# Kernel tuning notes

Measured on AMD Instinct MI355X. Metric: run time of the kernel, lower is better.

The kernel has to match this reference:

```python
import jax, jax.numpy as jnp
import numpy as np
import math

B, P, N = 4, 8, 512
D_MODEL, H, D_K = 128, 4, 32
T_ALL = 4
WHICH_IDX = np.array([0, 1, 3])  # which_transition_matrices = [T,T,F,T]
T = 3
EPS = 1e-5


def setup_inputs() -> dict:
    key = jax.random.key(0)
    ks = jax.random.split(key, 12)
    inputs = jax.random.normal(ks[0], (B, P, N, D_MODEL), jnp.float32)
    c_inputs = jax.random.normal(ks[1], (B, P, N, D_MODEL), jnp.float32)
    vals = jax.random.uniform(ks[2], (T_ALL, N, N), jnp.float32)
    keep = (jax.random.uniform(ks[3], (T_ALL, N, N)) < 0.05).astype(jnp.float32)
    eye = jnp.eye(N, dtype=jnp.float32)
    transition_matrices = vals * keep * (1.0 - eye) + eye
    s = 1.0 / math.sqrt(D_MODEL)
    Wq = jax.random.normal(ks[4], (T, D_MODEL, D_MODEL), jnp.float32) * s
    Wk = jax.random.normal(ks[5], (T, D_MODEL, D_MODEL), jnp.float32) * s
    Wv = jax.random.normal(ks[6], (T, D_MODEL, D_MODEL), jnp.float32) * s
    Wo = jax.random.normal(ks[7], (D_MODEL, T * D_MODEL), jnp.float32) * (1.0 / math.sqrt(T * D_MODEL))
    ln_gamma = jnp.ones((D_MODEL,), jnp.float32)
    ln_beta = jnp.zeros((D_MODEL,), jnp.float32)
    return dict(inputs=inputs, c_inputs=c_inputs, transition_matrices=transition_matrices,
                Wq=Wq, Wk=Wk, Wv=Wv, Wo=Wo, ln_gamma=ln_gamma, ln_beta=ln_beta)


def reference(inputs, c_inputs, transition_matrices, Wq, Wk, Wv, Wo, ln_gamma, ln_beta):
    tm = transition_matrices[jnp.asarray(WHICH_IDX)]  # [T, N, N]
    # per-transition-matrix projections (torch Linear: x @ W.T), then split heads
    def proj(W):
        y = jnp.einsum('bpnd,tod->tbpno', inputs, W)
        return y.reshape(T, B, P, N, H, D_K)
    Q, K, V = proj(Wq), proj(Wk), proj(Wv)
    scores = jnp.einsum('tbpnhk,tbpmhk->tbphnm', Q, K) / math.sqrt(D_K)
    mask = jnp.where(tm != 0, 0.0, -jnp.inf)[:, None, None, None]  # [T,1,1,1,N,N]
    alpha = jax.nn.softmax(scores + mask, axis=-1)
    # post-softmax reweighting by transition matrix, then V matmul
    out = jnp.einsum('tbphnm,tbpmhk->tbpnhk', alpha * tm[:, None, None, None], V)
    out = out.reshape(T, B, P, N, D_MODEL)
    out = jnp.moveaxis(out, 0, -2).reshape(B, P, N, T * D_MODEL)  # concat over matrices
    out = jnp.einsum('bpnf,df->bpnd', out, Wo)  # final Linear (bias=False); dropout p=0
    res = out + inputs
    mu = res.mean(-1, keepdims=True)
    var = ((res - mu) ** 2).mean(-1, keepdims=True)
    return (res - mu) / jnp.sqrt(var + EPS) * ln_gamma + ln_beta
```

## Files before the change

kernel.cpp:

```cpp
#include <hip/hip_runtime.h>


typedef __attribute__((ext_vector_type(8))) short  short8;
typedef __attribute__((ext_vector_type(4))) float  floatx4;

#define WS_BIG   50331648ull
#define WS_XL    54919168ull
#define QSCALE   0.25503486f

__device__ __forceinline__ float b2f(unsigned short u) {
    union { unsigned int i; float f; } v; v.i = ((unsigned int)u) << 16; return v.f;
}
__device__ __forceinline__ unsigned short f2b(float f) {
    union { float f; unsigned int i; } v; v.f = f;
    unsigned int x = v.i;
    return (unsigned short)((x + 0x7fffu + ((x >> 16) & 1u)) >> 16);
}
__device__ __forceinline__ short8 cvt8(const float* p) {
    floatx4 a = *(const floatx4*)p;
    floatx4 b = *(const floatx4*)(p + 4);
    short8 r;
    r[0] = (short)f2b(a[0]); r[1] = (short)f2b(a[1]);
    r[2] = (short)f2b(a[2]); r[3] = (short)f2b(a[3]);
    r[4] = (short)f2b(b[0]); r[5] = (short)f2b(b[1]);
    r[6] = (short)f2b(b[2]); r[7] = (short)f2b(b[3]);
    return r;
}

__global__ __launch_bounds__(256) void k_prep(
    const float* __restrict__ X,  const float* __restrict__ Wq,
    const float* __restrict__ Wk, const float* __restrict__ Wv,
    const float* __restrict__ Wo,
    unsigned short* __restrict__ Xb, unsigned short* __restrict__ Wb,
    unsigned short* __restrict__ Wob)
{
    size_t i = ((size_t)blockIdx.x * 256 + threadIdx.x) * 8;
    const float* src; unsigned short* dst; size_t off;
    if      (i < 2097152) { src = X;  dst = Xb;          off = i; }
    else if (i < 2146304) { src = Wq; dst = Wb;          off = i - 2097152; }
    else if (i < 2195456) { src = Wk; dst = Wb + 49152;  off = i - 2146304; }
    else if (i < 2244608) { src = Wv; dst = Wb + 98304;  off = i - 2195456; }
    else                  { src = Wo; dst = Wob;         off = i - 2244608; }
    *(short8*)&dst[off] = cvt8(&src[off]);
}

__global__ __launch_bounds__(256) void k_qkv_pre(
    const unsigned short* __restrict__ Xb,
    const unsigned short* __restrict__ Wb,
    unsigned short* __restrict__ q_ws,
    unsigned short* __restrict__ k_ws,
    unsigned short* __restrict__ v_ws)
{
    int bp = blockIdx.x, mt = blockIdx.y, tz = blockIdx.z;
    __shared__ unsigned short Xs[128 * 128];
    __shared__ unsigned short Cs[4][32 * 128];
    int tid = threadIdx.x;
    int lane = tid & 63, wv = tid >> 6;
    int l15 = lane & 15, quad = lane >> 4;

    const unsigned short* Xbase = Xb + ((size_t)bp * 512 + mt * 128) * 128;
    for (int i = 0; i < 8; ++i) {
        int e = (i * 256 + tid) * 8;
        *(short8*)&Xs[e] = *(const short8*)&Xbase[e];
    }
    __syncthreads();

    unsigned short* Osel[3] = { q_ws, k_ws, v_ws };
    int rt0 = wv * 2, rt1 = wv * 2 + 1;

    for (int qkv = 0; qkv < 3; ++qkv) {
        const unsigned short* Wt = Wb + qkv * 49152 + tz * 16384;
        unsigned short* Ob = Osel[qkv] + (size_t)tz * 2097152
                           + ((size_t)bp * 512 + mt * 128 + wv * 32) * 128;
        float sc = (qkv == 0) ? QSCALE : 1.0f;

        for (int ct = 0; ct < 8; ++ct) {
            short8 bfr[4];
            for (int kk = 0; kk < 4; ++kk)
                bfr[kk] = *(const short8*)&Wt[(size_t)(ct * 16 + l15) * 128 + kk * 32 + quad * 8];
            floatx4 acc0 = {0.f, 0.f, 0.f, 0.f};
            floatx4 acc1 = {0.f, 0.f, 0.f, 0.f};
            for (int kk = 0; kk < 4; ++kk) {
                short8 a0 = *(const short8*)&Xs[(rt0 * 16 + l15) * 128 + kk * 32 + quad * 8];
                short8 a1 = *(const short8*)&Xs[(rt1 * 16 + l15) * 128 + kk * 32 + quad * 8];
                acc0 = __builtin_amdgcn_mfma_f32_16x16x32_bf16(a0, bfr[kk], acc0, 0, 0, 0);
                acc1 = __builtin_amdgcn_mfma_f32_16x16x32_bf16(a1, bfr[kk], acc1, 0, 0, 0);
            }
            #pragma unroll
            for (int i = 0; i < 4; ++i) {
                int row = quad * 4 + i;
                int swz = (row & 7) << 4;
                int col = (ct * 16 + l15) ^ swz;
                Cs[wv][row * 128 + col]        = f2b(acc0[i] * sc);
                Cs[wv][(16 + row) * 128 + col] = f2b(acc1[i] * sc);
            }
        }
        #pragma unroll
        for (int j = 0; j < 8; ++j) {
            int flat = j * 64 + lane;
            int r = flat >> 4;
            int cg = (flat & 15) * 8;
            int cgs = cg ^ ((r & 7) << 4);
            *(short8*)&Ob[(size_t)r * 128 + cg] = *(const short8*)&Cs[wv][r * 128 + cgs];
        }
    }
}

__global__ __launch_bounds__(256) void k_qkv_cvt(
    const float* __restrict__ X,
    const float* __restrict__ Wq, const float* __restrict__ Wk,
    const float* __restrict__ Wv,
    unsigned short* __restrict__ q_ws, unsigned short* __restrict__ k_ws,
    unsigned short* __restrict__ v_ws,
    int wstride, int ostride)
{
    int bp = blockIdx.x, mt = blockIdx.y, tz = blockIdx.z;
    __shared__ unsigned short Xs[128 * 128];
    int tid = threadIdx.x;
    int lane = tid & 63, wv = tid >> 6;
    int l15 = lane & 15, quad = lane >> 4;

    const float* Xbase = X + ((size_t)bp * 512 + mt * 128) * 128;
    for (int i = 0; i < 8; ++i) {
        int e = (i * 256 + tid) * 8;
        *(short8*)&Xs[e] = cvt8(&Xbase[e]);
    }
    __syncthreads();

    size_t woff = (size_t)tz * wstride;
    size_t ooff = (size_t)tz * ostride;
    const float* Wsel[3] = { Wq + woff, Wk + woff, Wv + woff };
    unsigned short* Osel[3] = { q_ws + ooff, k_ws + ooff, v_ws + ooff };

    for (int qkv = 0; qkv < 3; ++qkv) {
        const float* Wt = Wsel[qkv];
        unsigned short* Ob = Osel[qkv] + ((size_t)bp * 512 + mt * 128) * 128;
        float sc = (qkv == 0) ? QSCALE : 1.0f;
        for (int ct = 0; ct < 8; ++ct) {
            short8 bfr[4];
            for (int kk = 0; kk < 4; ++kk)
                bfr[kk] = cvt8(&Wt[(size_t)(ct * 16 + l15) * 128 + kk * 32 + quad * 8]);
            floatx4 acc0 = {0.f, 0.f, 0.f, 0.f};
            floatx4 acc1 = {0.f, 0.f, 0.f, 0.f};
            int rt0 = wv * 2, rt1 = wv * 2 + 1;
            for (int kk = 0; kk < 4; ++kk) {
                short8 a0 = *(const short8*)&Xs[(rt0 * 16 + l15) * 128 + kk * 32 + quad * 8];
                short8 a1 = *(const short8*)&Xs[(rt1 * 16 + l15) * 128 + kk * 32 + quad * 8];
                acc0 = __builtin_amdgcn_mfma_f32_16x16x32_bf16(a0, bfr[kk], acc0, 0, 0, 0);
                acc1 = __builtin_amdgcn_mfma_f32_16x16x32_bf16(a1, bfr[kk], acc1, 0, 0, 0);
            }
            int col = ct * 16 + l15;
            for (int i = 0; i < 4; ++i) {
                Ob[(size_t)(rt0 * 16 + quad * 4 + i) * 128 + col] = f2b(acc0[i] * sc);
                Ob[(size_t)(rt1 * 16 + quad * 4 + i) * 128 + col] = f2b(acc1[i] * sc);
            }
        }
    }
}

__global__ __launch_bounds__(512) void k_attn(
    const unsigned short* __restrict__ q_ws,
    const unsigned short* __restrict__ k_ws,
    const unsigned short* __restrict__ v_ws,
    const float* __restrict__ tm,
    unsigned short* __restrict__ att_ws,
    int qkv_stride, int toff0)
{
    int nc = blockIdx.x;
    int bp = blockIdx.y;
    int z  = blockIdx.z;
    int t = z >> 2, h = z & 3;
    size_t qoff = (size_t)t * (size_t)qkv_stride;
    const float* tmt = tm + (size_t)(t + (t >> 1)) * 262144;
    int toff = toff0 + t * 128;

    __shared__ unsigned short Vt[32][516];
    __shared__ unsigned short Ps[8][16][72];

    int tid = threadIdx.x, lane = tid & 63, wv = tid >> 6;
    int l15 = lane & 15, quad = lane >> 4;

    {
        const unsigned short* vp = v_ws + qoff + ((size_t)bp * 512 + tid) * 128 + h * 32;
        short8 a = *(const short8*)vp;
        short8 b = *(const short8*)(vp + 8);
        short8 c = *(const short8*)(vp + 16);
        short8 d = *(const short8*)(vp + 24);
        #pragma unroll
        for (int j = 0; j < 8; ++j) {
            Vt[j][tid]      = (unsigned short)a[j];
            Vt[8 + j][tid]  = (unsigned short)b[j];
            Vt[16 + j][tid] = (unsigned short)c[j];
            Vt[24 + j][tid] = (unsigned short)d[j];
        }
    }
    int n0 = nc * 128 + wv * 16;
    short8 qf = *(const short8*)&q_ws[qoff +
        ((size_t)bp * 512 + n0 + l15) * 128 + h * 32 + quad * 8];
    __syncthreads();

    const unsigned short* Kb = k_ws + qoff + (size_t)bp * 512 * 128 + h * 32;
    floatx4 O0 = {0.f, 0.f, 0.f, 0.f};
    floatx4 O1 = {0.f, 0.f, 0.f, 0.f};
    float za[4] = {0.f, 0.f, 0.f, 0.f};
    const floatx4 zero4 = {0.f, 0.f, 0.f, 0.f};

    for (int c = 0; c < 8; ++c) {
        int mb = c * 64;
        short8 kf0 = *(const short8*)&Kb[(size_t)(mb +  0 + l15) * 128 + quad * 8];
        short8 kf1 = *(const short8*)&Kb[(size_t)(mb + 16 + l15) * 128 + quad * 8];
        short8 kf2 = *(const short8*)&Kb[(size_t)(mb + 32 + l15) * 128 + quad * 8];
        short8 kf3 = *(const short8*)&Kb[(size_t)(mb + 48 + l15) * 128 + quad * 8];
        floatx4 S[4];
        S[0] = __builtin_amdgcn_mfma_f32_16x16x32_bf16(qf, kf0, zero4, 0, 0, 0);
        S[1] = __builtin_amdgcn_mfma_f32_16x16x32_bf16(qf, kf1, zero4, 0, 0, 0);
        S[2] = __builtin_amdgcn_mfma_f32_16x16x32_bf16(qf, kf2, zero4, 0, 0, 0);
        S[3] = __builtin_amdgcn_mfma_f32_16x16x32_bf16(qf, kf3, zero4, 0, 0, 0);

        #pragma unroll
        for (int ti = 0; ti < 4; ++ti) {
            int m = mb + ti * 16 + l15;
            #pragma unroll
            for (int i = 0; i < 4; ++i) {
                float tmv = tmt[(size_t)(n0 + quad * 4 + i) * 512 + m];
                float e = __builtin_amdgcn_exp2f(S[ti][i]);
                bool on = (tmv != 0.0f);
                za[i] += on ? e : 0.0f;
                float w = on ? e * tmv : 0.0f;
                Ps[wv][quad * 4 + i][ti * 16 + l15] = f2b(w);
            }
        }
        #pragma unroll
        for (int kc = 0; kc < 2; ++kc) {
            short8 pa  = *(const short8*)&Ps[wv][l15][kc * 32 + quad * 8];
            short8 vb0 = *(const short8*)&Vt[l15][mb + kc * 32 + quad * 8];
            short8 vb1 = *(const short8*)&Vt[16 + l15][mb + kc * 32 + quad * 8];
            O0 = __builtin_amdgcn_mfma_f32_16x16x32_bf16(pa, vb0, O0, 0, 0, 0);
            O1 = __builtin_amdgcn_mfma_f32_16x16x32_bf16(pa, vb1, O1, 0, 0, 0);
        }
    }

    #pragma unroll
    for (int d = 1; d < 16; d <<= 1) {
        #pragma unroll
        for (int i = 0; i < 4; ++i) za[i] += __shfl_xor(za[i], d, 64);
    }
    #pragma unroll
    for (int i = 0; i < 4; ++i) {
        float rz = 1.0f / za[i];
        size_t row = (size_t)bp * 512 + n0 + quad * 4 + i;
        att_ws[row * 384 + toff + h * 32 + l15]      = f2b(O0[i] * rz);
        att_ws[row * 384 + toff + h * 32 + 16 + l15] = f2b(O1[i] * rz);
    }
}

__global__ __launch_bounds__(256) void k_oproj_pre(
    const unsigned short* __restrict__ att_ws,
    const unsigned short* __restrict__ Wob,
    const float* __restrict__ X,
    const float* __restrict__ gamma,
    const float* __restrict__ beta,
    float* __restrict__ out)
{
    int bp = blockIdx.x;
    int mt = blockIdx.y;
    __shared__ unsigned short As[64 * 128];
    __shared__ unsigned short Ws[128 * 128];
    int tid = threadIdx.x, lane = tid & 63, wv = tid >> 6;
    int l15 = lane & 15, quad = lane >> 4;

    floatx4 acc[8];
    for (int ct = 0; ct < 8; ++ct) acc[ct] = (floatx4){0.f, 0.f, 0.f, 0.f};
    size_t rowbase = (size_t)bp * 512 + mt * 64;

    for (int kc = 0; kc < 3; ++kc) {
        __syncthreads();
        for (int i = 0; i < 4; ++i) {
            int flat = i * 256 + tid;
            int row = flat >> 4, colg = (flat & 15) * 8;
            *(short8*)&As[row * 128 + colg] =
                *(const short8*)&att_ws[(rowbase + row) * 384 + kc * 128 + colg];
        }
        for (int i = 0; i < 8; ++i) {
            int flat = i * 256 + tid;
            int row = flat >> 4, colg = (flat & 15) * 8;
            *(short8*)&Ws[row * 128 + colg] =
                *(const short8*)&Wob[(size_t)row * 384 + kc * 128 + colg];
        }
        __syncthreads();
        for (int ct = 0; ct < 8; ++ct) {
            for (int kk = 0; kk < 4; ++kk) {
                short8 a = *(const short8*)&As[(wv * 16 + l15) * 128 + kk * 32 + quad * 8];
                short8 b = *(const short8*)&Ws[(ct * 16 + l15) * 128 + kk * 32 + quad * 8];
                acc[ct] = __builtin_amdgcn_mfma_f32_16x16x32_bf16(a, b, acc[ct], 0, 0, 0);
            }
        }
    }

    for (int i = 0; i < 4; ++i) {
        int lrow = wv * 16 + quad * 4 + i;
        size_t grow = rowbase + lrow;
        float vals[8];
        float s = 0.f, sq = 0.f;
        for (int ct = 0; ct < 8; ++ct) {
            int col = ct * 16 + l15;
            float v = acc[ct][i] + X[grow * 128 + col];
            vals[ct] = v;
            s += v; sq += v * v;
        }
        for (int d = 1; d < 16; d <<= 1) {
            s  += __shfl_xor(s, d, 64);
            sq += __shfl_xor(sq, d, 64);
        }
        float mu = s * (1.0f / 128.0f);
        float var = sq * (1.0f / 128.0f) - mu * mu;
        float rs = rsqrtf(var + 1e-5f);
        for (int ct = 0; ct < 8; ++ct) {
            int col = ct * 16 + l15;
            out[grow * 128 + col] = (vals[ct] - mu) * rs * gamma[col] + beta[col];
        }
    }
}

__global__ __launch_bounds__(256) void k_oproj_cvt(
    const unsigned short* __restrict__ att_ws,
    const float* __restrict__ Wo,
    const float* __restrict__ X,
    const float* __restrict__ gamma,
    const float* __restrict__ beta,
    float* __restrict__ out)
{
    int bp = blockIdx.x;
    int mt = blockIdx.y;
    __shared__ unsigned short As[64 * 128];
    __shared__ unsigned short Ws[128 * 128];
    int tid = threadIdx.x, lane = tid & 63, wv = tid >> 6;
    int l15 = lane & 15, quad = lane >> 4;

    floatx4 acc[8];
    for (int ct = 0; ct < 8; ++ct) acc[ct] = (floatx4){0.f, 0.f, 0.f, 0.f};
    size_t rowbase = (size_t)bp * 512 + mt * 64;

    for (int kc = 0; kc < 3; ++kc) {
        __syncthreads();
        for (int i = 0; i < 4; ++i) {
            int flat = i * 256 + tid;
            int row = flat >> 4, colg = (flat & 15) * 8;
            *(short8*)&As[row * 128 + colg] =
                *(const short8*)&att_ws[(rowbase + row) * 384 + kc * 128 + colg];
        }
        for (int i = 0; i < 8; ++i) {
            int flat = i * 256 + tid;
            int row = flat >> 4, colg = (flat & 15) * 8;
            *(short8*)&Ws[row * 128 + colg] = cvt8(&Wo[(size_t)row * 384 + kc * 128 + colg]);
        }
        __syncthreads();
        for (int ct = 0; ct < 8; ++ct) {
            for (int kk = 0; kk < 4; ++kk) {
                short8 a = *(const short8*)&As[(wv * 16 + l15) * 128 + kk * 32 + quad * 8];
                short8 b = *(const short8*)&Ws[(ct * 16 + l15) * 128 + kk * 32 + quad * 8];
                acc[ct] = __builtin_amdgcn_mfma_f32_16x16x32_bf16(a, b, acc[ct], 0, 0, 0);
            }
        }
    }

    for (int i = 0; i < 4; ++i) {
        int lrow = wv * 16 + quad * 4 + i;
        size_t grow = rowbase + lrow;
        float vals[8];
        float s = 0.f, sq = 0.f;
        for (int ct = 0; ct < 8; ++ct) {
            int col = ct * 16 + l15;
            float v = acc[ct][i] + X[grow * 128 + col];
            vals[ct] = v;
            s += v; sq += v * v;
        }
        for (int d = 1; d < 16; d <<= 1) {
            s  += __shfl_xor(s, d, 64);
            sq += __shfl_xor(sq, d, 64);
        }
        float mu = s * (1.0f / 128.0f);
        float var = sq * (1.0f / 128.0f) - mu * mu;
        float rs = rsqrtf(var + 1e-5f);
        for (int ct = 0; ct < 8; ++ct) {
            int col = ct * 16 + l15;
            out[grow * 128 + col] = (vals[ct] - mu) * rs * gamma[col] + beta[col];
        }
    }
}

extern "C" void kernel_launch(void* const* d_in, const int* in_sizes, int n_in,
                              void* d_out, int out_size, void* d_ws, size_t ws_size,
                              hipStream_t stream) {
    const float* X     = (const float*)d_in[0];
    const float* TM    = (const float*)d_in[2];
    const float* Wq    = (const float*)d_in[3];
    const float* Wk    = (const float*)d_in[4];
    const float* Wv    = (const float*)d_in[5];
    const float* Wo    = (const float*)d_in[6];
    const float* gamma = (const float*)d_in[7];
    const float* beta  = (const float*)d_in[8];
    float* out = (float*)d_out;

    char* ws = (char*)d_ws;
    const size_t QKV1 = 2097152;
    const size_t QKV1B = QKV1 * 2;

    if (ws_size >= WS_XL) {
        unsigned short* q3  = (unsigned short*)(ws);
        unsigned short* k3  = (unsigned short*)(ws + 3 * QKV1B);
        unsigned short* v3  = (unsigned short*)(ws + 6 * QKV1B);
        unsigned short* att = (unsigned short*)(ws + 9 * QKV1B);
        unsigned short* Xb  = (unsigned short*)(ws + 50331648ull);
        unsigned short* Wb  = (unsigned short*)(ws + 54525952ull);
        unsigned short* Wob = (unsigned short*)(ws + 54820864ull);
        k_prep<<<dim3(1120), 256, 0, stream>>>(X, Wq, Wk, Wv, Wo, Xb, Wb, Wob);
        k_qkv_pre<<<dim3(32, 4, 3), 256, 0, stream>>>(Xb, Wb, q3, k3, v3);
        k_attn<<<dim3(4, 32, 12), 512, 0, stream>>>(q3, k3, v3, TM, att, (int)QKV1, 0);
        k_oproj_pre<<<dim3(32, 8), 256, 0, stream>>>(att, Wob, X, gamma, beta, out);
    } else if (ws_size >= WS_BIG) {
        unsigned short* q3  = (unsigned short*)(ws);
        unsigned short* k3  = (unsigned short*)(ws + 3 * QKV1B);
        unsigned short* v3  = (unsigned short*)(ws + 6 * QKV1B);
        unsigned short* att = (unsigned short*)(ws + 9 * QKV1B);
        k_qkv_cvt<<<dim3(32, 4, 3), 256, 0, stream>>>(
            X, Wq, Wk, Wv, q3, k3, v3, 16384, (int)QKV1);
        k_attn<<<dim3(4, 32, 12), 512, 0, stream>>>(q3, k3, v3, TM, att, (int)QKV1, 0);
        k_oproj_cvt<<<dim3(32, 8), 256, 0, stream>>>(att, Wo, X, gamma, beta, out);
    } else {
        unsigned short* q_ws   = (unsigned short*)(ws);
        unsigned short* k_ws   = (unsigned short*)(ws + QKV1B);
        unsigned short* v_ws   = (unsigned short*)(ws + 2 * QKV1B);
        unsigned short* att_ws = (unsigned short*)(ws + 3 * QKV1B);
        const int tsel[3] = {0, 1, 3};
        for (int t = 0; t < 3; ++t) {
            k_qkv_cvt<<<dim3(32, 4, 1), 256, 0, stream>>>(
                X, Wq + (size_t)t * 16384, Wk + (size_t)t * 16384, Wv + (size_t)t * 16384,
                q_ws, k_ws, v_ws, 0, 0);
            k_attn<<<dim3(4, 32, 4), 512, 0, stream>>>(
                q_ws, k_ws, v_ws, TM + (size_t)tsel[t] * 262144, att_ws, 0, t * 128);
        }
        k_oproj_cvt<<<dim3(32, 8), 256, 0, stream>>>(att_ws, Wo, X, gamma, beta, out);
    }
}
```

Baseline: 187.7 us.

## Process two query tiles per attention block to reuse K fragments and V transpose

Each attention block now handles 256 query rows instead of 128, with each wave holding two Q fragments and reusing the loaded K fragments and the shared-memory transposed V for both. This halves the grid along the query axis, so the per-block V transpose and K global loads are amortized over twice the work. It also drops the mask select on the weight (since tm is zero where masked) and switches to a cheaper round-half-up bf16 conversion for P. In exchange there is more register pressure, fewer blocks for occupancy and latency hiding, and slightly different rounding.

```diff
diff --git a/kernel.cpp b/kernel.cpp
--- a/kernel.cpp
+++ b/kernel.cpp
@@ -15,6 +15,9 @@
     union { float f; unsigned int i; } v; v.f = f;
     unsigned int x = v.i;
     return (unsigned short)((x + 0x7fffu + ((x >> 16) & 1u)) >> 16);
+}
+__device__ __forceinline__ unsigned int fbits(float f) {
+    union { float f; unsigned int i; } v; v.f = f; return v.i;
 }
 __device__ __forceinline__ short8 cvt8(const float* p) {
     floatx4 a = *(const floatx4*)p;
@@ -158,7 +161,7 @@
     }
 }
 
-__global__ __launch_bounds__(512) void k_attn(
+__global__ __launch_bounds__(512) void k_attn2(
     const unsigned short* __restrict__ q_ws,
     const unsigned short* __restrict__ k_ws,
     const unsigned short* __restrict__ v_ws,
@@ -166,7 +169,7 @@
     unsigned short* __restrict__ att_ws,
     int qkv_stride, int toff0)
 {
-    int nc = blockIdx.x;
+    int nc2 = blockIdx.x;
     int bp = blockIdx.y;
     int z  = blockIdx.z;
     int t = z >> 2, h = z & 3;
@@ -194,15 +197,18 @@
             Vt[24 + j][tid] = (unsigned short)d[j];
         }
     }
-    int n0 = nc * 128 + wv * 16;
-    short8 qf = *(const short8*)&q_ws[qoff +
+    int n0 = nc2 * 256 + wv * 16;
+    short8 qf[2];
+    qf[0] = *(const short8*)&q_ws[qoff +
         ((size_t)bp * 512 + n0 + l15) * 128 + h * 32 + quad * 8];
+    qf[1] = *(const short8*)&q_ws[qoff +
+        ((size_t)bp * 512 + n0 + 128 + l15) * 128 + h * 32 + quad * 8];
     __syncthreads();
 
     const unsigned short* Kb = k_ws + qoff + (size_t)bp * 512 * 128 + h * 32;
-    floatx4 O0 = {0.f, 0.f, 0.f, 0.f};
-    floatx4 O1 = {0.f, 0.f, 0.f, 0.f};
-    float za[4] = {0.f, 0.f, 0.f, 0.f};
+    floatx4 O0[2] = {{0.f,0.f,0.f,0.f},{0.f,0.f,0.f,0.f}};
+    floatx4 O1[2] = {{0.f,0.f,0.f,0.f},{0.f,0.f,0.f,0.f}};
+    float za[2][4] = {{0.f,0.f,0.f,0.f},{0.f,0.f,0.f,0.f}};
     const floatx4 zero4 = {0.f, 0.f, 0.f, 0.f};
 
     for (int c = 0; c < 8; ++c) {
@@ -211,46 +217,54 @@
         short8 kf1 = *(const short8*)&Kb[(size_t)(mb + 16 + l15) * 128 + quad * 8];
         short8 kf2 = *(const short8*)&Kb[(size_t)(mb + 32 + l15) * 128 + quad * 8];
         short8 kf3 = *(const short8*)&Kb[(size_t)(mb + 48 + l15) * 128 + quad * 8];
-        floatx4 S[4];
-        S[0] = __builtin_amdgcn_mfma_f32_16x16x32_bf16(qf, kf0, zero4, 0, 0, 0);
-        S[1] = __builtin_amdgcn_mfma_f32_16x16x32_bf16(qf, kf1, zero4, 0, 0, 0);
-        S[2] = __builtin_amdgcn_mfma_f32_16x16x32_bf16(qf, kf2, zero4, 0, 0, 0);
-        S[3] = __builtin_amdgcn_mfma_f32_16x16x32_bf16(qf, kf3, zero4, 0, 0, 0);
 
         #pragma unroll
-        for (int ti = 0; ti < 4; ++ti) {
-            int m = mb + ti * 16 + l15;
+        for (int s = 0; s < 2; ++s) {
+            int ns = n0 + s * 128;
+            floatx4 S[4];
+            S[0] = __builtin_amdgcn_mfma_f32_16x16x32_bf16(qf[s], kf0, zero4, 0, 0, 0);
+            S[1] = __builtin_amdgcn_mfma_f32_16x16x32_bf16(qf[s], kf1, zero4, 0, 0, 0);
+            S[2] = __builtin_amdgcn_mfma_f32_16x16x32_bf16(qf[s], kf2, zero4, 0, 0, 0);
+            S[3] = __builtin_amdgcn_mfma_f32_16x16x32_bf16(qf[s], kf3, zero4, 0, 0, 0);
+
             #pragma unroll
-            for (int i = 0; i < 4; ++i) {
-                float tmv = tmt[(size_t)(n0 + quad * 4 + i) * 512 + m];
-                float e = __builtin_amdgcn_exp2f(S[ti][i]);
-                bool on = (tmv != 0.0f);
-                za[i] += on ? e : 0.0f;
-                float w = on ? e * tmv : 0.0f;
-                Ps[wv][quad * 4 + i][ti * 16 + l15] = f2b(w);
-            }
-        }
+            for (int ti = 0; ti < 4; ++ti) {
+                int m = mb + ti * 16 + l15;
+                #pragma unroll
+                for (int i = 0; i < 4; ++i) {
+                    float tmv = tmt[(size_t)(ns + quad * 4 + i) * 512 + m];
+                    float e = __builtin_amdgcn_exp2f(S[ti][i]);
+                    za[s][i] += (tmv != 0.0f) ? e : 0.0f;
+                    float w = e * tmv;
+                    Ps[wv][quad * 4 + i][ti * 16 + l15] =
+                        (unsigned short)((fbits(w) + 0x8000u) >> 16);
+                }
+            }
+            #pragma unroll
+            for (int kc = 0; kc < 2; ++kc) {
+                short8 pa  = *(const short8*)&Ps[wv][l15][kc * 32 + quad * 8];
+                short8 vb0 = *(const short8*)&Vt[l15][mb + kc * 32 + quad * 8];
+                short8 vb1 = *(const short8*)&Vt[16 + l15][mb + kc * 32 + quad * 8];
+                O0[s] = __builtin_amdgcn_mfma_f32_16x16x32_bf16(pa, vb0, O0[s], 0, 0, 0);
+                O1[s] = __builtin_amdgcn_mfma_f32_16x16x32_bf16(pa, vb1, O1[s], 0, 0, 0);
+            }
+        }
+    }
+
+    #pragma unroll
+    for (int s = 0; s < 2; ++s) {
         #pragma unroll
-        for (int kc = 0; kc < 2; ++kc) {
-            short8 pa  = *(const short8*)&Ps[wv][l15][kc * 32 + quad * 8];
-            short8 vb0 = *(const short8*)&Vt[l15][mb + kc * 32 + quad * 8];
-            short8 vb1 = *(const short8*)&Vt[16 + l15][mb + kc * 32 + quad * 8];
-            O0 = __builtin_amdgcn_mfma_f32_16x16x32_bf16(pa, vb0, O0, 0, 0, 0);
-            O1 = __builtin_amdgcn_mfma_f32_16x16x32_bf16(pa, vb1, O1, 0, 0, 0);
-        }
-    }
-
-    #pragma unroll
-    for (int d = 1; d < 16; d <<= 1) {
+        for (int d = 1; d < 16; d <<= 1) {
+            #pragma unroll
+            for (int i = 0; i < 4; ++i) za[s][i] += __shfl_xor(za[s][i], d, 64);
+        }
         #pragma unroll
-        for (int i = 0; i < 4; ++i) za[i] += __shfl_xor(za[i], d, 64);
-    }
-    #pragma unroll
-    for (int i = 0; i < 4; ++i) {
-        float rz = 1.0f / za[i];
-        size_t row = (size_t)bp * 512 + n0 + quad * 4 + i;
-        att_ws[row * 384 + toff + h * 32 + l15]      = f2b(O0[i] * rz);
-        att_ws[row * 384 + toff + h * 32 + 16 + l15] = f2b(O1[i] * rz);
+        for (int i = 0; i < 4; ++i) {
+            float rz = 1.0f / za[s][i];
+            size_t row = (size_t)bp * 512 + n0 + s * 128 + quad * 4 + i;
+            att_ws[row * 384 + toff + h * 32 + l15]      = f2b(O0[s][i] * rz);
+            att_ws[row * 384 + toff + h * 32 + 16 + l15] = f2b(O1[s][i] * rz);
+        }
     }
 }
 
@@ -416,7 +430,7 @@
         unsigned short* Wob = (unsigned short*)(ws + 54820864ull);
         k_prep<<<dim3(1120), 256, 0, stream>>>(X, Wq, Wk, Wv, Wo, Xb, Wb, Wob);
         k_qkv_pre<<<dim3(32, 4, 3), 256, 0, stream>>>(Xb, Wb, q3, k3, v3);
-        k_attn<<<dim3(4, 32, 12), 512, 0, stream>>>(q3, k3, v3, TM, att, (int)QKV1, 0);
+        k_attn2<<<dim3(2, 32, 12), 512, 0, stream>>>(q3, k3, v3, TM, att, (int)QKV1, 0);
         k_oproj_pre<<<dim3(32, 8), 256, 0, stream>>>(att, Wob, X, gamma, beta, out);
     } else if (ws_size >= WS_BIG) {
         unsigned short* q3  = (unsigned short*)(ws);
@@ -425,7 +439,7 @@
         unsigned short* att = (unsigned short*)(ws + 9 * QKV1B);
         k_qkv_cvt<<<dim3(32, 4, 3), 256, 0, stream>>>(
             X, Wq, Wk, Wv, q3, k3, v3, 16384, (int)QKV1);
-        k_attn<<<dim3(4, 32, 12), 512, 0, stream>>>(q3, k3, v3, TM, att, (int)QKV1, 0);
+        k_attn2<<<dim3(2, 32, 12), 512, 0, stream>>>(q3, k3, v3, TM, att, (int)QKV1, 0);
         k_oproj_cvt<<<dim3(32, 8), 256, 0, stream>>>(att, Wo, X, gamma, beta, out);
     } else {
         unsigned short* q_ws   = (unsigned short*)(ws);
@@ -437,7 +451,7 @@
             k_qkv_cvt<<<dim3(32, 4, 1), 256, 0, stream>>>(
                 X, Wq + (size_t)t * 16384, Wk + (size_t)t * 16384, Wv + (size_t)t * 16384,
                 q_ws, k_ws, v_ws, 0, 0);
-            k_attn<<<dim3(4, 32, 4), 512, 0, stream>>>(
+            k_attn2<<<dim3(2, 32, 4), 512, 0, stream>>>(
                 q_ws, k_ws, v_ws, TM + (size_t)tsel[t] * 262144, att_ws, 0, t * 128);
         }
         k_oproj_cvt<<<dim3(32, 8), 256, 0, stream>>>(att_ws, Wo, X, gamma, beta, out);
```

After: 171.4 us. 8.7% less time.
